# Optimization experiments

Measured on AMD Instinct MI355X. Metric: run time of the kernel, lower is better.

## Reference

```python
import jax, jax.numpy as jnp
import numpy as np

B, N, D = 2, 256, 128
LN_EPS = 1e-5


def _linear_params(key, d, scale):
    kw, kb = jax.random.split(key)
    W = jax.random.normal(kw, (d, d), jnp.float32) * scale
    b = jax.random.normal(kb, (d,), jnp.float32) * 0.02
    return W, b


def setup_inputs() -> dict:
    key = jax.random.key(0)
    ks = jax.random.split(key, 8)
    hidden_states = jax.random.normal(ks[0], (B, N, D), jnp.float32)
    structure_matrix = jax.random.normal(ks[1], (B, N, N, D), jnp.float32)
    scale = 1.0 / np.sqrt(D).astype(np.float32)
    Wq, bq = _linear_params(ks[2], D, scale)
    Wk, bk = _linear_params(ks[3], D, scale)
    Wv, bv = _linear_params(ks[4], D, scale)
    Wo, bo = _linear_params(ks[5], D, scale)
    ln_g = jnp.ones((D,), jnp.float32)
    ln_b = jnp.zeros((D,), jnp.float32)
    return dict(hidden_states=hidden_states, structure_matrix=structure_matrix,
                Wq=Wq, bq=bq, Wk=Wk, bk=bk, Wv=Wv, bv=bv, Wo=Wo, bo=bo,
                ln_g=ln_g, ln_b=ln_b)


def reference(hidden_states, structure_matrix, Wq, bq, Wk, bk, Wv, bv, Wo, bo, ln_g, ln_b):
    # hidden_states is accepted by the original forward but never used.
    d = structure_matrix.shape[-1]
    q = structure_matrix @ Wq + bq  # [B,N,N,D]
    k = structure_matrix @ Wk + bk
    v = structure_matrix @ Wv + bv
    # scores[b,i,j,k] = <Q[b,i,k,:], K[b,i,j,:]> / sqrt(D)
    # (equivalent to the torch broadcast multiply+sum, expressed as batched GEMM)
    scores = jnp.einsum('bikd,bijd->bijk', q, k) / jnp.sqrt(jnp.asarray(d, scores_dtype := q.dtype))
    probs = jax.nn.relu(scores)  # dropout is identity in eval mode
    # context[b,i,j,d] = sum_k probs[b,i,j,k] * V[b,i,k,d]
    ctx = jnp.einsum('bijk,bikd->bijd', probs, v)
    out = ctx @ Wo + bo
    x = out + structure_matrix  # residual
    mu = jnp.mean(x, axis=-1, keepdims=True)
    var = jnp.var(x, axis=-1, keepdims=True)
    return (x - mu) * jax.lax.rsqrt(var + LN_EPS) * ln_g + ln_b
```

## Files before the change

kernel.cpp:

```cpp
#include <hip/hip_runtime.h>

#define DEV static __device__ __forceinline__

typedef __bf16 bf16x8 __attribute__((ext_vector_type(8)));
typedef float  f32x16 __attribute__((ext_vector_type(16)));

DEV int rowmap(int r, int hi) { return (r & 3) + 8 * (r >> 2) + 4 * hi; }

DEV int swzQ(int row, int col) {
  return row * 256 + (((((col >> 3) ^ (row & 15)) << 3) | (col & 7)) << 1);
}
DEV int swzV(int d, int k) {
  return d * 512 + (((((k >> 3) ^ (d & 31)) << 3) | (k & 7)) << 1);
}

DEV unsigned pack2(float lo, float hi) {
  union { __bf16 h[2]; unsigned u; } x;
  x.h[0] = (__bf16)lo; x.h[1] = (__bf16)hi;
  return x.u;
}

DEV bf16x8 mk_frag(float d0, float d1, float d2, float d3,
                   float d4, float d5, float d6, float d7, int lane) {
  unsigned a0 = pack2(d0, d1), a1 = pack2(d2, d3);
  unsigned b0 = pack2(d4, d5), b1 = pack2(d6, d7);
  unsigned a0s = __shfl_xor(a0, 32), a1s = __shfl_xor(a1, 32);
  unsigned b0s = __shfl_xor(b0, 32), b1s = __shfl_xor(b1, 32);
  bool lo = lane < 32;
  union { unsigned u[4]; bf16x8 v; } r;
  r.u[0] = lo ? a0  : b0s;
  r.u[1] = lo ? a1  : b1s;
  r.u[2] = lo ? a0s : b0;
  r.u[3] = lo ? a1s : b1;
  return r.v;
}

DEV f32x16 fzero() {
  f32x16 z;
  #pragma unroll
  for (int i = 0; i < 16; ++i) z[i] = 0.f;
  return z;
}

DEV void gld16(const char* g, char* l) {
  __builtin_amdgcn_global_load_lds(
      (const __attribute__((address_space(1))) void*)g,
      (__attribute__((address_space(3))) void*)l, 16, 0, 0);
}

DEV void stage_w32(const float* __restrict__ W, char* dst, int tid) {
  #pragma unroll
  for (int it = 0; it < 32; ++it) {
    int idx = tid + it * 512;
    int e = idx >> 7, dp = idx & 127;
    *reinterpret_cast<__bf16*>(dst + swzQ(dp, e)) = (__bf16)W[idx];
  }
}

__global__ void prep_wt(const float* __restrict__ Wk, const float* __restrict__ Wq,
                        const float* __restrict__ Wv, const float* __restrict__ Wo,
                        __bf16* __restrict__ wt) {
  int idx = blockIdx.x * 256 + threadIdx.x;
  const float* W[4] = {Wk, Wq, Wv, Wo};
  int m = idx >> 14, rem = idx & 16383;
  int e = rem >> 7, dp = rem & 127;
  wt[m * 16384 + (swzQ(dp, e) >> 1)] = (__bf16)W[m][rem];
}

template<bool WS>
__global__ __launch_bounds__(512, 2)
void sapd_fused(const float* __restrict__ S,
                const float* __restrict__ bq, const float* __restrict__ bk,
                const float* __restrict__ bv, const float* __restrict__ bo,
                const float* __restrict__ Wq, const float* __restrict__ Wk,
                const float* __restrict__ Wv, const float* __restrict__ Wo,
                const float* __restrict__ lg, const float* __restrict__ lb,
                const __bf16* __restrict__ wt,
                float* __restrict__ out)
{
  extern __shared__ char smem[];
  char* RA = smem;
  char* RB = smem + 65536;

  const int tid  = threadIdx.x;
  const int lane = tid & 63;
  const int w    = tid >> 6;
  const int ml   = lane & 31;
  const int hi   = lane >> 5;
  const size_t sbase = (size_t)blockIdx.x * (256 * 128);
  const char* wsc = (const char*)wt;

  if (WS) {
    #pragma unroll
    for (int j = 0; j < 12; ++j) {
      int c = w + 8 * j;
      char* dst = (c < 64) ? (RB + c * 1024) : (RA + (c - 64) * 1024);
      gld16(wsc + c * 1024 + lane * 16, dst);
    }
  } else {
    stage_w32(Wk, RB, tid);
    stage_w32(Wq, RB + 32768, tid);
    stage_w32(Wv, RA, tid);
  }

  bf16x8 sfrag[8];
  {
    const float* srow = S + sbase + (size_t)(32 * w + ml) * 128;
    #pragma unroll
    for (int kk = 0; kk < 8; ++kk) {
      float4 a = *reinterpret_cast<const float4*>(srow + 16 * kk + 8 * hi);
      float4 b = *reinterpret_cast<const float4*>(srow + 16 * kk + 8 * hi + 4);
      bf16x8 f;
      f[0] = (__bf16)a.x; f[1] = (__bf16)a.y; f[2] = (__bf16)a.z; f[3] = (__bf16)a.w;
      f[4] = (__bf16)b.x; f[5] = (__bf16)b.y; f[6] = (__bf16)b.z; f[7] = (__bf16)b.w;
      sfrag[kk] = f;
    }
  }
  __syncthreads();

  bf16x8 kfrag[8];
  {
    f32x16 accK[4];
    #pragma unroll
    for (int t = 0; t < 4; ++t) accK[t] = fzero();
    #pragma unroll
    for (int kk = 0; kk < 8; ++kk) {
      #pragma unroll
      for (int t = 0; t < 4; ++t) {
        bf16x8 wf = *reinterpret_cast<const bf16x8*>(
            RB + swzQ(32 * t + ml, 16 * kk + 8 * hi));
        accK[t] = __builtin_amdgcn_mfma_f32_32x32x16_bf16(wf, sfrag[kk], accK[t], 0, 0, 0);
      }
    }
    #pragma unroll
    for (int t = 0; t < 4; ++t) {
      #pragma unroll
      for (int r = 0; r < 16; ++r) accK[t][r] += bk[32 * t + rowmap(r, hi)];
      kfrag[2 * t]     = mk_frag(accK[t][0], accK[t][1], accK[t][2], accK[t][3],
                                 accK[t][4], accK[t][5], accK[t][6], accK[t][7], lane);
      kfrag[2 * t + 1] = mk_frag(accK[t][8], accK[t][9], accK[t][10], accK[t][11],
                                 accK[t][12], accK[t][13], accK[t][14], accK[t][15], lane);
    }
  }

  {
    f32x16 accV[4];
    #pragma unroll
    for (int t = 0; t < 4; ++t) accV[t] = fzero();
    #pragma unroll
    for (int kk = 0; kk < 8; ++kk) {
      #pragma unroll
      for (int t = 0; t < 4; ++t) {
        bf16x8 wf = *reinterpret_cast<const bf16x8*>(
            RA + swzQ(32 * t + ml, 16 * kk + 8 * hi));
        accV[t] = __builtin_amdgcn_mfma_f32_32x32x16_bf16(sfrag[kk], wf, accV[t], 0, 0, 0);
      }
    }
    __syncthreads();
    #pragma unroll
    for (int t = 0; t < 4; ++t) {
      float bb = bv[32 * t + ml];
      int d = 32 * t + ml;
      #pragma unroll
      for (int p = 0; p < 8; ++p) {
        int k = 32 * w + rowmap(2 * p, hi);
        *reinterpret_cast<unsigned*>(RA + swzV(d, k)) =
            pack2(accV[t][2 * p] + bb, accV[t][2 * p + 1] + bb);
      }
    }
  }

  {
    f32x16 accQ[4];
    #pragma unroll
    for (int t = 0; t < 4; ++t) accQ[t] = fzero();
    #pragma unroll
    for (int kk = 0; kk < 8; ++kk) {
      #pragma unroll
      for (int t = 0; t < 4; ++t) {
        bf16x8 wf = *reinterpret_cast<const bf16x8*>(
            RB + 32768 + swzQ(32 * t + ml, 16 * kk + 8 * hi));
        accQ[t] = __builtin_amdgcn_mfma_f32_32x32x16_bf16(sfrag[kk], wf, accQ[t], 0, 0, 0);
      }
    }
    __syncthreads();
    #pragma unroll
    for (int t = 0; t < 4; ++t) {
      float bb = bq[32 * t + ml];
      #pragma unroll
      for (int r = 0; r < 16; ++r)
        *reinterpret_cast<__bf16*>(
            RB + swzQ(32 * w + rowmap(r, hi), 32 * t + ml)) =
            (__bf16)(accQ[t][r] + bb);
    }
  }
  __syncthreads();

  f32x16 ctx[4];
  #pragma unroll
  for (int m = 0; m < 4; ++m) ctx[m] = fzero();
  const float SC = 0.088388347648318447f;

  #pragma unroll 2
  for (int kt = 0; kt < 8; ++kt) {
    f32x16 sa = fzero();
    __builtin_amdgcn_s_setprio(1);
    #pragma unroll
    for (int kk = 0; kk < 8; ++kk) {
      bf16x8 qf = *reinterpret_cast<const bf16x8*>(
          RB + swzQ(32 * kt + ml, 16 * kk + 8 * hi));
      sa = __builtin_amdgcn_mfma_f32_32x32x16_bf16(qf, kfrag[kk], sa, 0, 0, 0);
    }
    __builtin_amdgcn_s_setprio(0);
    float p[16];
    #pragma unroll
    for (int r = 0; r < 16; ++r) p[r] = fmaxf(sa[r] * SC, 0.f);
    bf16x8 pf0 = mk_frag(p[0], p[1], p[2], p[3], p[4], p[5], p[6], p[7], lane);
    bf16x8 pf1 = mk_frag(p[8], p[9], p[10], p[11], p[12], p[13], p[14], p[15], lane);
    __builtin_amdgcn_s_setprio(1);
    #pragma unroll
    for (int m = 0; m < 4; ++m) {
      bf16x8 vf0 = *reinterpret_cast<const bf16x8*>(
          RA + swzV(32 * m + ml, 32 * kt + 8 * hi));
      ctx[m] = __builtin_amdgcn_mfma_f32_32x32x16_bf16(vf0, pf0, ctx[m], 0, 0, 0);
      bf16x8 vf1 = *reinterpret_cast<const bf16x8*>(
          RA + swzV(32 * m + ml, 32 * kt + 16 + 8 * hi));
      ctx[m] = __builtin_amdgcn_mfma_f32_32x32x16_bf16(vf1, pf1, ctx[m], 0, 0, 0);
    }
    __builtin_amdgcn_s_setprio(0);

    if (kt == 3) {
      __syncthreads();
      if (WS) {
        #pragma unroll
        for (int j = 0; j < 4; ++j) {
          int c = w + 8 * j;
          gld16(wsc + 98304 + c * 1024 + lane * 16, RB + c * 1024);
        }
      } else {
        stage_w32(Wo, RB, tid);
      }
    }
  }

  bf16x8 cf[8];
  #pragma unroll
  for (int m = 0; m < 4; ++m) {
    cf[2 * m]     = mk_frag(ctx[m][0], ctx[m][1], ctx[m][2], ctx[m][3],
                            ctx[m][4], ctx[m][5], ctx[m][6], ctx[m][7], lane);
    cf[2 * m + 1] = mk_frag(ctx[m][8], ctx[m][9], ctx[m][10], ctx[m][11],
                            ctx[m][12], ctx[m][13], ctx[m][14], ctx[m][15], lane);
  }
  float resv[4][16];
  #pragma unroll
  for (int t = 0; t < 4; ++t) {
    #pragma unroll
    for (int r = 0; r < 16; ++r)
      resv[t][r] = S[sbase + (size_t)(32 * w + rowmap(r, hi)) * 128 + 32 * t + ml];
  }
  __syncthreads();

  f32x16 oa[4];
  #pragma unroll
  for (int t = 0; t < 4; ++t) oa[t] = fzero();
  #pragma unroll
  for (int kk = 0; kk < 8; ++kk) {
    #pragma unroll
    for (int t = 0; t < 4; ++t) {
      bf16x8 wf = *reinterpret_cast<const bf16x8*>(
          RB + swzQ(32 * t + ml, 16 * kk + 8 * hi));
      oa[t] = __builtin_amdgcn_mfma_f32_32x32x16_bf16(cf[kk], wf, oa[t], 0, 0, 0);
    }
  }

  float gg[4], lbv[4], bov[4];
  #pragma unroll
  for (int t = 0; t < 4; ++t) {
    gg[t]  = lg[32 * t + ml];
    lbv[t] = lb[32 * t + ml];
    bov[t] = bo[32 * t + ml];
  }
  float sum[16], ssq[16];
  #pragma unroll
  for (int r = 0; r < 16; ++r) { sum[r] = 0.f; ssq[r] = 0.f; }
  #pragma unroll
  for (int t = 0; t < 4; ++t) {
    #pragma unroll
    for (int r = 0; r < 16; ++r) {
      float x = oa[t][r] + bov[t] + resv[t][r];
      oa[t][r] = x;
      sum[r] += x;
      ssq[r] += x * x;
    }
  }
  #pragma unroll
  for (int r = 0; r < 16; ++r) {
    float s_ = sum[r], q_ = ssq[r];
    #pragma unroll
    for (int m = 1; m <= 16; m <<= 1) {
      s_ += __shfl_xor(s_, m);
      q_ += __shfl_xor(q_, m);
    }
    float mu = s_ * (1.f / 128.f);
    float var = q_ * (1.f / 128.f) - mu * mu;
    float rs = rsqrtf(var + 1e-5f);
    float* orow = out + sbase + (size_t)(32 * w + rowmap(r, hi)) * 128;
    #pragma unroll
    for (int t = 0; t < 4; ++t)
      orow[32 * t + ml] = (oa[t][r] - mu) * rs * gg[t] + lbv[t];
  }
}

extern "C" void kernel_launch(void* const* d_in, const int* in_sizes, int n_in,
                              void* d_out, int out_size, void* d_ws, size_t ws_size,
                              hipStream_t stream) {
  (void)in_sizes; (void)n_in; (void)out_size;
  const float* S  = (const float*)d_in[1];
  const float* Wq = (const float*)d_in[2];
  const float* bq = (const float*)d_in[3];
  const float* Wk = (const float*)d_in[4];
  const float* bk = (const float*)d_in[5];
  const float* Wv = (const float*)d_in[6];
  const float* bv = (const float*)d_in[7];
  const float* Wo = (const float*)d_in[8];
  const float* bo = (const float*)d_in[9];
  const float* lg = (const float*)d_in[10];
  const float* lb = (const float*)d_in[11];
  float* out = (float*)d_out;

  constexpr int SMEM = 131072;
  bool use_ws = (d_ws != nullptr) && (ws_size >= 131072);
  if (use_ws) {
    prep_wt<<<dim3(256), dim3(256), 0, stream>>>(Wk, Wq, Wv, Wo, (__bf16*)d_ws);
    (void)hipFuncSetAttribute(reinterpret_cast<const void*>(&sapd_fused<true>),
                              hipFuncAttributeMaxDynamicSharedMemorySize, SMEM);
    sapd_fused<true><<<dim3(512), dim3(512), SMEM, stream>>>(
        S, bq, bk, bv, bo, Wq, Wk, Wv, Wo, lg, lb, (const __bf16*)d_ws, out);
  } else {
    (void)hipFuncSetAttribute(reinterpret_cast<const void*>(&sapd_fused<false>),
                              hipFuncAttributeMaxDynamicSharedMemorySize, SMEM);
    sapd_fused<false><<<dim3(512), dim3(512), SMEM, stream>>>(
        S, bq, bk, bv, bo, Wq, Wk, Wv, Wo, lg, lb, nullptr, out);
  }
}
```

Measured before the change: 72.79 us.

## Split each row tile across two waves with 1024-thread blocks

Result: slower. 144.0 us (+97.8%).

```diff
diff --git a/kernel.cpp b/kernel.cpp
--- a/kernel.cpp
+++ b/kernel.cpp
@@ -19,6 +19,8 @@
   x.h[0] = (__bf16)lo; x.h[1] = (__bf16)hi;
   return x.u;
 }
+DEV float bflo(unsigned u) { union { unsigned u; float f; } x; x.u = u << 16;        return x.f; }
+DEV float bfhi(unsigned u) { union { unsigned u; float f; } x; x.u = u & 0xffff0000u; return x.f; }
 
 DEV bf16x8 mk_frag(float d0, float d1, float d2, float d3,
                    float d4, float d5, float d6, float d7, int lane) {
@@ -50,8 +52,8 @@
 
 DEV void stage_w32(const float* __restrict__ W, char* dst, int tid) {
   #pragma unroll
-  for (int it = 0; it < 32; ++it) {
-    int idx = tid + it * 512;
+  for (int it = 0; it < 16; ++it) {
+    int idx = tid + it * 1024;
     int e = idx >> 7, dp = idx & 127;
     *reinterpret_cast<__bf16*>(dst + swzQ(dp, e)) = (__bf16)W[idx];
   }
@@ -68,7 +70,7 @@
 }
 
 template<bool WS>
-__global__ __launch_bounds__(512, 2)
+__global__ __launch_bounds__(1024, 4)
 void sapd_fused(const float* __restrict__ S,
                 const float* __restrict__ bq, const float* __restrict__ bk,
                 const float* __restrict__ bv, const float* __restrict__ bo,
@@ -85,6 +87,8 @@
   const int tid  = threadIdx.x;
   const int lane = tid & 63;
   const int w    = tid >> 6;
+  const int p    = w >> 1;
+  const int s    = w & 1;
   const int ml   = lane & 31;
   const int hi   = lane >> 5;
   const size_t sbase = (size_t)blockIdx.x * (256 * 128);
@@ -92,20 +96,22 @@
 
   if (WS) {
     #pragma unroll
-    for (int j = 0; j < 12; ++j) {
-      int c = w + 8 * j;
-      char* dst = (c < 64) ? (RB + c * 1024) : (RA + (c - 64) * 1024);
+    for (int jj = 0; jj < 6; ++jj) {
+      int c = w + 16 * jj;
+      char* dst = (c < 32) ? (RA + c * 1024)
+                : (c < 64) ? (RB + (c - 32) * 1024)
+                           : (RA + 32768 + (c - 64) * 1024);
       gld16(wsc + c * 1024 + lane * 16, dst);
     }
   } else {
-    stage_w32(Wk, RB, tid);
-    stage_w32(Wq, RB + 32768, tid);
-    stage_w32(Wv, RA, tid);
+    stage_w32(Wk, RA, tid);
+    stage_w32(Wq, RB, tid);
+    stage_w32(Wv, RA + 32768, tid);
   }
 
   bf16x8 sfrag[8];
   {
-    const float* srow = S + sbase + (size_t)(32 * w + ml) * 128;
+    const float* srow = S + sbase + (size_t)(32 * p + ml) * 128;
     #pragma unroll
     for (int kk = 0; kk < 8; ++kk) {
       float4 a = *reinterpret_cast<const float4*>(srow + 16 * kk + 8 * hi);
@@ -128,7 +134,7 @@
       #pragma unroll
       for (int t = 0; t < 4; ++t) {
         bf16x8 wf = *reinterpret_cast<const bf16x8*>(
-            RB + swzQ(32 * t + ml, 16 * kk + 8 * hi));
+            RA + swzQ(32 * t + ml, 16 * kk + 8 * hi));
         accK[t] = __builtin_amdgcn_mfma_f32_32x32x16_bf16(wf, sfrag[kk], accK[t], 0, 0, 0);
       }
     }
@@ -143,56 +149,54 @@
     }
   }
 
-  {
-    f32x16 accV[4];
-    #pragma unroll
-    for (int t = 0; t < 4; ++t) accV[t] = fzero();
-    #pragma unroll
-    for (int kk = 0; kk < 8; ++kk) {
-      #pragma unroll
-      for (int t = 0; t < 4; ++t) {
-        bf16x8 wf = *reinterpret_cast<const bf16x8*>(
-            RA + swzQ(32 * t + ml, 16 * kk + 8 * hi));
-        accV[t] = __builtin_amdgcn_mfma_f32_32x32x16_bf16(sfrag[kk], wf, accV[t], 0, 0, 0);
-      }
-    }
-    __syncthreads();
-    #pragma unroll
-    for (int t = 0; t < 4; ++t) {
-      float bb = bv[32 * t + ml];
-      int d = 32 * t + ml;
-      #pragma unroll
-      for (int p = 0; p < 8; ++p) {
-        int k = 32 * w + rowmap(2 * p, hi);
-        *reinterpret_cast<unsigned*>(RA + swzV(d, k)) =
-            pack2(accV[t][2 * p] + bb, accV[t][2 * p + 1] + bb);
-      }
-    }
-  }
-
-  {
-    f32x16 accQ[4];
-    #pragma unroll
-    for (int t = 0; t < 4; ++t) accQ[t] = fzero();
-    #pragma unroll
-    for (int kk = 0; kk < 8; ++kk) {
-      #pragma unroll
-      for (int t = 0; t < 4; ++t) {
-        bf16x8 wf = *reinterpret_cast<const bf16x8*>(
-            RB + 32768 + swzQ(32 * t + ml, 16 * kk + 8 * hi));
-        accQ[t] = __builtin_amdgcn_mfma_f32_32x32x16_bf16(sfrag[kk], wf, accQ[t], 0, 0, 0);
-      }
-    }
-    __syncthreads();
-    #pragma unroll
-    for (int t = 0; t < 4; ++t) {
-      float bb = bq[32 * t + ml];
-      #pragma unroll
-      for (int r = 0; r < 16; ++r)
-        *reinterpret_cast<__bf16*>(
-            RB + swzQ(32 * w + rowmap(r, hi), 32 * t + ml)) =
-            (__bf16)(accQ[t][r] + bb);
-    }
+  f32x16 accV[2];
+  accV[0] = fzero(); accV[1] = fzero();
+  #pragma unroll
+  for (int kk = 0; kk < 8; ++kk) {
+    #pragma unroll
+    for (int tt = 0; tt < 2; ++tt) {
+      int t = 2 * s + tt;
+      bf16x8 wf = *reinterpret_cast<const bf16x8*>(
+          RA + 32768 + swzQ(32 * t + ml, 16 * kk + 8 * hi));
+      accV[tt] = __builtin_amdgcn_mfma_f32_32x32x16_bf16(sfrag[kk], wf, accV[tt], 0, 0, 0);
+    }
+  }
+
+  f32x16 accQ[2];
+  accQ[0] = fzero(); accQ[1] = fzero();
+  #pragma unroll
+  for (int kk = 0; kk < 8; ++kk) {
+    #pragma unroll
+    for (int tt = 0; tt < 2; ++tt) {
+      int t = 2 * s + tt;
+      bf16x8 wf = *reinterpret_cast<const bf16x8*>(
+          RB + swzQ(32 * t + ml, 16 * kk + 8 * hi));
+      accQ[tt] = __builtin_amdgcn_mfma_f32_32x32x16_bf16(sfrag[kk], wf, accQ[tt], 0, 0, 0);
+    }
+  }
+  __syncthreads();
+
+  #pragma unroll
+  for (int tt = 0; tt < 2; ++tt) {
+    int t = 2 * s + tt;
+    float bb = bv[32 * t + ml];
+    int d = 32 * t + ml;
+    #pragma unroll
+    for (int q = 0; q < 8; ++q) {
+      int k = 32 * p + rowmap(2 * q, hi);
+      *reinterpret_cast<unsigned*>(RA + swzV(d, k)) =
+          pack2(accV[tt][2 * q] + bb, accV[tt][2 * q + 1] + bb);
+    }
+  }
+  #pragma unroll
+  for (int tt = 0; tt < 2; ++tt) {
+    int t = 2 * s + tt;
+    float bb = bq[32 * t + ml];
+    #pragma unroll
+    for (int r = 0; r < 16; ++r)
+      *reinterpret_cast<__bf16*>(
+          RB + swzQ(32 * p + rowmap(r, hi), 32 * t + ml)) =
+          (__bf16)(accQ[tt][r] + bb);
   }
   __syncthreads();
 
@@ -201,8 +205,9 @@
   for (int m = 0; m < 4; ++m) ctx[m] = fzero();
   const float SC = 0.088388347648318447f;
 
-  #pragma unroll 2
-  for (int kt = 0; kt < 8; ++kt) {
+  #pragma unroll
+  for (int c = 0; c < 4; ++c) {
+    int kt = 4 * s + c;
     f32x16 sa = fzero();
     __builtin_amdgcn_s_setprio(1);
     #pragma unroll
@@ -212,11 +217,11 @@
       sa = __builtin_amdgcn_mfma_f32_32x32x16_bf16(qf, kfrag[kk], sa, 0, 0, 0);
     }
     __builtin_amdgcn_s_setprio(0);
-    float p[16];
-    #pragma unroll
-    for (int r = 0; r < 16; ++r) p[r] = fmaxf(sa[r] * SC, 0.f);
-    bf16x8 pf0 = mk_frag(p[0], p[1], p[2], p[3], p[4], p[5], p[6], p[7], lane);
-    bf16x8 pf1 = mk_frag(p[8], p[9], p[10], p[11], p[12], p[13], p[14], p[15], lane);
+    float pv[16];
+    #pragma unroll
+    for (int r = 0; r < 16; ++r) pv[r] = fmaxf(sa[r] * SC, 0.f);
+    bf16x8 pf0 = mk_frag(pv[0], pv[1], pv[2], pv[3], pv[4], pv[5], pv[6], pv[7], lane);
+    bf16x8 pf1 = mk_frag(pv[8], pv[9], pv[10], pv[11], pv[12], pv[13], pv[14], pv[15], lane);
     __builtin_amdgcn_s_setprio(1);
     #pragma unroll
     for (int m = 0; m < 4; ++m) {
@@ -228,17 +233,62 @@
       ctx[m] = __builtin_amdgcn_mfma_f32_32x32x16_bf16(vf1, pf1, ctx[m], 0, 0, 0);
     }
     __builtin_amdgcn_s_setprio(0);
-
-    if (kt == 3) {
-      __syncthreads();
-      if (WS) {
-        #pragma unroll
-        for (int j = 0; j < 4; ++j) {
-          int c = w + 8 * j;
-          gld16(wsc + 98304 + c * 1024 + lane * 16, RB + c * 1024);
-        }
-      } else {
-        stage_w32(Wo, RB, tid);
+  }
+  __syncthreads();
+
+  if (WS) {
+    #pragma unroll
+    for (int jj = 0; jj < 2; ++jj) {
+      int c = w + 16 * jj;
+      gld16(wsc + 98304 + c * 1024 + lane * 16, RB + c * 1024);
+    }
+  } else {
+    stage_w32(Wo, RB, tid);
+  }
+  char* XC = RA + p * 8192;
+  if (s == 1) {
+    #pragma unroll
+    for (int m = 0; m < 4; ++m) {
+      #pragma unroll
+      for (int q = 0; q < 8; ++q) {
+        int d2 = (32 * m + rowmap(2 * q, hi)) >> 1;
+        *reinterpret_cast<unsigned*>(XC + d2 * 128 + ml * 4) =
+            pack2(ctx[m][2 * q], ctx[m][2 * q + 1]);
+      }
+    }
+  }
+  __syncthreads();
+  if (s == 0) {
+    #pragma unroll
+    for (int m = 0; m < 4; ++m) {
+      #pragma unroll
+      for (int q = 0; q < 8; ++q) {
+        int d2 = (32 * m + rowmap(2 * q, hi)) >> 1;
+        unsigned u = *reinterpret_cast<unsigned*>(XC + d2 * 128 + ml * 4);
+        ctx[m][2 * q]     += bflo(u);
+        ctx[m][2 * q + 1] += bfhi(u);
+      }
+    }
+    #pragma unroll
+    for (int m = 0; m < 4; ++m) {
+      #pragma unroll
+      for (int q = 0; q < 8; ++q) {
+        int d2 = (32 * m + rowmap(2 * q, hi)) >> 1;
+        *reinterpret_cast<unsigned*>(XC + d2 * 128 + ml * 4) =
+            pack2(ctx[m][2 * q], ctx[m][2 * q + 1]);
+      }
+    }
+  }
+  __syncthreads();
+  if (s == 1) {
+    #pragma unroll
+    for (int m = 0; m < 4; ++m) {
+      #pragma unroll
+      for (int q = 0; q < 8; ++q) {
+        int d2 = (32 * m + rowmap(2 * q, hi)) >> 1;
+        unsigned u = *reinterpret_cast<unsigned*>(XC + d2 * 128 + ml * 4);
+        ctx[m][2 * q]     = bflo(u);
+        ctx[m][2 * q + 1] = bfhi(u);
       }
     }
   }
@@ -251,48 +301,50 @@
     cf[2 * m + 1] = mk_frag(ctx[m][8], ctx[m][9], ctx[m][10], ctx[m][11],
                             ctx[m][12], ctx[m][13], ctx[m][14], ctx[m][15], lane);
   }
-  float resv[4][16];
-  #pragma unroll
-  for (int t = 0; t < 4; ++t) {
+  float resv[2][16];
+  #pragma unroll
+  for (int tt = 0; tt < 2; ++tt) {
     #pragma unroll
     for (int r = 0; r < 16; ++r)
-      resv[t][r] = S[sbase + (size_t)(32 * w + rowmap(r, hi)) * 128 + 32 * t + ml];
-  }
-  __syncthreads();
-
-  f32x16 oa[4];
-  #pragma unroll
-  for (int t = 0; t < 4; ++t) oa[t] = fzero();
+      resv[tt][r] = S[sbase + (size_t)(32 * p + rowmap(r, hi)) * 128 +
+                      32 * (2 * s + tt) + ml];
+  }
+
+  f32x16 oa[2];
+  oa[0] = fzero(); oa[1] = fzero();
   #pragma unroll
   for (int kk = 0; kk < 8; ++kk) {
     #pragma unroll
-    for (int t = 0; t < 4; ++t) {
+    for (int tt = 0; tt < 2; ++tt) {
+      int t = 2 * s + tt;
       bf16x8 wf = *reinterpret_cast<const bf16x8*>(
           RB + swzQ(32 * t + ml, 16 * kk + 8 * hi));
-      oa[t] = __builtin_amdgcn_mfma_f32_32x32x16_bf16(cf[kk], wf, oa[t], 0, 0, 0);
-    }
-  }
-
-  float gg[4], lbv[4], bov[4];
-  #pragma unroll
-  for (int t = 0; t < 4; ++t) {
-    gg[t]  = lg[32 * t + ml];
-    lbv[t] = lb[32 * t + ml];
-    bov[t] = bo[32 * t + ml];
+      oa[tt] = __builtin_amdgcn_mfma_f32_32x32x16_bf16(cf[kk], wf, oa[tt], 0, 0, 0);
+    }
+  }
+
+  float gg[2], lbv[2], bov[2];
+  #pragma unroll
+  for (int tt = 0; tt < 2; ++tt) {
+    int t = 2 * s + tt;
+    gg[tt]  = lg[32 * t + ml];
+    lbv[tt] = lb[32 * t + ml];
+    bov[tt] = bo[32 * t + ml];
   }
   float sum[16], ssq[16];
   #pragma unroll
   for (int r = 0; r < 16; ++r) { sum[r] = 0.f; ssq[r] = 0.f; }
   #pragma unroll
-  for (int t = 0; t < 4; ++t) {
+  for (int tt = 0; tt < 2; ++tt) {
     #pragma unroll
     for (int r = 0; r < 16; ++r) {
-      float x = oa[t][r] + bov[t] + resv[t][r];
-      oa[t][r] = x;
+      float x = oa[tt][r] + bov[tt] + resv[tt][r];
+      oa[tt][r] = x;
       sum[r] += x;
       ssq[r] += x * x;
     }
   }
+  char* SX = RB + 32768;
   #pragma unroll
   for (int r = 0; r < 16; ++r) {
     float s_ = sum[r], q_ = ssq[r];
@@ -301,13 +353,24 @@
       s_ += __shfl_xor(s_, m);
       q_ += __shfl_xor(q_, m);
     }
-    float mu = s_ * (1.f / 128.f);
-    float var = q_ * (1.f / 128.f) - mu * mu;
+    if (ml == 0) {
+      float2 v; v.x = s_; v.y = q_;
+      *reinterpret_cast<float2*>(SX + p * 512 + rowmap(r, hi) * 16 + s * 8) = v;
+    }
+  }
+  __syncthreads();
+  #pragma unroll
+  for (int r = 0; r < 16; ++r) {
+    int row = rowmap(r, hi);
+    float2 a = *reinterpret_cast<float2*>(SX + p * 512 + row * 16);
+    float2 b = *reinterpret_cast<float2*>(SX + p * 512 + row * 16 + 8);
+    float mu = (a.x + b.x) * (1.f / 128.f);
+    float var = (a.y + b.y) * (1.f / 128.f) - mu * mu;
     float rs = rsqrtf(var + 1e-5f);
-    float* orow = out + sbase + (size_t)(32 * w + rowmap(r, hi)) * 128;
-    #pragma unroll
-    for (int t = 0; t < 4; ++t)
-      orow[32 * t + ml] = (oa[t][r] - mu) * rs * gg[t] + lbv[t];
+    float* orow = out + sbase + (size_t)(32 * p + row) * 128;
+    #pragma unroll
+    for (int tt = 0; tt < 2; ++tt)
+      orow[32 * (2 * s + tt) + ml] = (oa[tt][r] - mu) * rs * gg[tt] + lbv[tt];
   }
 }
 
@@ -334,12 +397,12 @@
     prep_wt<<<dim3(256), dim3(256), 0, stream>>>(Wk, Wq, Wv, Wo, (__bf16*)d_ws);
     (void)hipFuncSetAttribute(reinterpret_cast<const void*>(&sapd_fused<true>),
                               hipFuncAttributeMaxDynamicSharedMemorySize, SMEM);
-    sapd_fused<true><<<dim3(512), dim3(512), SMEM, stream>>>(
+    sapd_fused<true><<<dim3(512), dim3(1024), SMEM, stream>>>(
         S, bq, bk, bv, bo, Wq, Wk, Wv, Wo, lg, lb, (const __bf16*)d_ws, out);
   } else {
     (void)hipFuncSetAttribute(reinterpret_cast<const void*>(&sapd_fused<false>),
                               hipFuncAttributeMaxDynamicSharedMemorySize, SMEM);
-    sapd_fused<false><<<dim3(512), dim3(512), SMEM, stream>>>(
+    sapd_fused<false><<<dim3(512), dim3(1024), SMEM, stream>>>(
         S, bq, bk, bv, bo, Wq, Wk, Wv, Wo, lg, lb, nullptr, out);
   }
 }
```

## Fold Q/K and V/O weight products algebraically to skip per-tile projections

Applied to the files above, without the earlier changes.

New measurement: 233.7 us. 221% more time.

```diff
diff --git a/kernel.cpp b/kernel.cpp
--- a/kernel.cpp
+++ b/kernel.cpp
@@ -9,9 +9,6 @@
 
 DEV int swzQ(int row, int col) {
   return row * 256 + (((((col >> 3) ^ (row & 15)) << 3) | (col & 7)) << 1);
-}
-DEV int swzV(int d, int k) {
-  return d * 512 + (((((k >> 3) ^ (d & 31)) << 3) | (k & 7)) << 1);
 }
 
 DEV unsigned pack2(float lo, float hi) {
@@ -48,39 +45,82 @@
       (__attribute__((address_space(3))) void*)l, 16, 0, 0);
 }
 
-DEV void stage_w32(const float* __restrict__ W, char* dst, int tid) {
-  #pragma unroll
-  for (int it = 0; it < 32; ++it) {
-    int idx = tid + it * 512;
-    int e = idx >> 7, dp = idx & 127;
-    *reinterpret_cast<__bf16*>(dst + swzQ(dp, e)) = (__bf16)W[idx];
-  }
-}
-
-__global__ void prep_wt(const float* __restrict__ Wk, const float* __restrict__ Wq,
-                        const float* __restrict__ Wv, const float* __restrict__ Wo,
-                        __bf16* __restrict__ wt) {
-  int idx = blockIdx.x * 256 + threadIdx.x;
-  const float* W[4] = {Wk, Wq, Wv, Wo};
-  int m = idx >> 14, rem = idx & 16383;
-  int e = rem >> 7, dp = rem & 127;
-  wt[m * 16384 + (swzQ(dp, e) >> 1)] = (__bf16)W[m][rem];
-}
-
-template<bool WS>
+DEV void st_write(char* SB, int colbase, const bf16x8 sf[8], int ml, int hi) {
+  #pragma unroll
+  for (int kk = 0; kk < 8; ++kk) {
+    union { bf16x8 v; unsigned u[4]; } o, q;
+    o.v = sf[kk];
+    #pragma unroll
+    for (int x = 0; x < 4; ++x) q.u[x] = __shfl_xor(o.u[x], 1);
+    bool even = ((ml & 1) == 0);
+    if (even ? (kk < 4) : (kk >= 4)) {
+      int col = colbase + (ml & ~1);
+      #pragma unroll
+      for (int i = 0; i < 8; ++i) {
+        int e = 16 * kk + 8 * hi + i;
+        union { __bf16 h[2]; unsigned u; } pk;
+        pk.h[0] = even ? o.v[i] : q.v[i];
+        pk.h[1] = even ? q.v[i] : o.v[i];
+        *reinterpret_cast<unsigned*>(SB + swzQ(e, col)) = pk.u;
+      }
+    }
+  }
+}
+
+__global__ void prep_mat(const float* __restrict__ X, const float* __restrict__ Y,
+                         char* __restrict__ dst, int transx) {
+  extern __shared__ char pm[];
+  float* yl = reinterpret_cast<float*>(pm);
+  float* xl = yl + 128 * 129;
+  int t = threadIdx.x;
+  int a0 = blockIdx.x * 16;
+  for (int i = t; i < 16384; i += 256) yl[(i >> 7) * 129 + (i & 127)] = Y[i];
+  for (int i = t; i < 2048; i += 256) {
+    int aa = i >> 7, d = i & 127;
+    xl[aa * 129 + d] = transx ? X[d * 128 + a0 + aa] : X[(a0 + aa) * 128 + d];
+  }
+  __syncthreads();
+  int b = t & 127, ah = t >> 7;
+  #pragma unroll
+  for (int aa = 0; aa < 8; ++aa) {
+    int a = ah * 8 + aa;
+    float acc = 0.f;
+    for (int d = 0; d < 128; ++d) acc += xl[a * 129 + d] * yl[b * 129 + d];
+    *reinterpret_cast<__bf16*>(dst + swzQ(a0 + a, b)) = (__bf16)acc;
+  }
+}
+
+__global__ void prep_v(const float* __restrict__ Wq, const float* __restrict__ Wk,
+                       const float* __restrict__ Wo,
+                       const float* __restrict__ bq, const float* __restrict__ bk,
+                       const float* __restrict__ bv, float* __restrict__ dstf) {
+  int e = threadIdx.x;
+  float a1 = 0.f, a2 = 0.f, a3 = 0.f;
+  for (int d = 0; d < 128; ++d) {
+    a1 += Wq[e * 128 + d] * bk[d];
+    a2 += Wk[e * 128 + d] * bq[d];
+    a3 += bv[d] * Wo[d * 128 + e];
+  }
+  dstf[e] = a1; dstf[128 + e] = a2; dstf[256 + e] = a3;
+  if (e == 0) {
+    float c = 0.f;
+    for (int d = 0; d < 128; ++d) c += bq[d] * bk[d];
+    dstf[384] = c;
+  }
+}
+
 __global__ __launch_bounds__(512, 2)
 void sapd_fused(const float* __restrict__ S,
-                const float* __restrict__ bq, const float* __restrict__ bk,
-                const float* __restrict__ bv, const float* __restrict__ bo,
-                const float* __restrict__ Wq, const float* __restrict__ Wk,
-                const float* __restrict__ Wv, const float* __restrict__ Wo,
+                const float* __restrict__ bo,
                 const float* __restrict__ lg, const float* __restrict__ lb,
-                const __bf16* __restrict__ wt,
+                const char* __restrict__ ws,
                 float* __restrict__ out)
 {
   extern __shared__ char smem[];
-  char* RA = smem;
-  char* RB = smem + 65536;
+  char* SA = smem;
+  char* SB = smem + 32768;
+  float* a_lds  = reinterpret_cast<float*>(smem + 65536);
+  float* rs_lds = a_lds + 256;
 
   const int tid  = threadIdx.x;
   const int lane = tid & 63;
@@ -88,19 +128,12 @@
   const int ml   = lane & 31;
   const int hi   = lane >> 5;
   const size_t sbase = (size_t)blockIdx.x * (256 * 128);
-  const char* wsc = (const char*)wt;
-
-  if (WS) {
-    #pragma unroll
-    for (int j = 0; j < 12; ++j) {
-      int c = w + 8 * j;
-      char* dst = (c < 64) ? (RB + c * 1024) : (RA + (c - 64) * 1024);
-      gld16(wsc + c * 1024 + lane * 16, dst);
-    }
-  } else {
-    stage_w32(Wk, RB, tid);
-    stage_w32(Wq, RB + 32768, tid);
-    stage_w32(Wv, RA, tid);
+  const float* wsf = reinterpret_cast<const float*>(ws + 65536);
+
+  #pragma unroll
+  for (int j = 0; j < 4; ++j) {
+    int c = w + 8 * j;
+    gld16(ws + c * 1024 + lane * 16, SA + c * 1024);
   }
 
   bf16x8 sfrag[8];
@@ -116,140 +149,144 @@
       sfrag[kk] = f;
     }
   }
-  __syncthreads();
-
-  bf16x8 kfrag[8];
+
+  if (w < 4) st_write(SB, 32 * w, sfrag, ml, hi);
+  __syncthreads();
+
+  bf16x8 rfrag[8];
   {
-    f32x16 accK[4];
-    #pragma unroll
-    for (int t = 0; t < 4; ++t) accK[t] = fzero();
+    f32x16 racc[4];
+    #pragma unroll
+    for (int t = 0; t < 4; ++t) racc[t] = fzero();
     #pragma unroll
     for (int kk = 0; kk < 8; ++kk) {
       #pragma unroll
       for (int t = 0; t < 4; ++t) {
-        bf16x8 wf = *reinterpret_cast<const bf16x8*>(
-            RB + swzQ(32 * t + ml, 16 * kk + 8 * hi));
-        accK[t] = __builtin_amdgcn_mfma_f32_32x32x16_bf16(wf, sfrag[kk], accK[t], 0, 0, 0);
+        bf16x8 gf = *reinterpret_cast<const bf16x8*>(
+            SA + swzQ(32 * t + ml, 16 * kk + 8 * hi));
+        racc[t] = __builtin_amdgcn_mfma_f32_32x32x16_bf16(gf, sfrag[kk], racc[t], 0, 0, 0);
       }
     }
     #pragma unroll
     for (int t = 0; t < 4; ++t) {
-      #pragma unroll
-      for (int r = 0; r < 16; ++r) accK[t][r] += bk[32 * t + rowmap(r, hi)];
-      kfrag[2 * t]     = mk_frag(accK[t][0], accK[t][1], accK[t][2], accK[t][3],
-                                 accK[t][4], accK[t][5], accK[t][6], accK[t][7], lane);
-      kfrag[2 * t + 1] = mk_frag(accK[t][8], accK[t][9], accK[t][10], accK[t][11],
-                                 accK[t][12], accK[t][13], accK[t][14], accK[t][15], lane);
-    }
-  }
-
+      rfrag[2 * t]     = mk_frag(racc[t][0], racc[t][1], racc[t][2], racc[t][3],
+                                 racc[t][4], racc[t][5], racc[t][6], racc[t][7], lane);
+      rfrag[2 * t + 1] = mk_frag(racc[t][8], racc[t][9], racc[t][10], racc[t][11],
+                                 racc[t][12], racc[t][13], racc[t][14], racc[t][15], lane);
+    }
+  }
+
+  float c_own;
   {
-    f32x16 accV[4];
-    #pragma unroll
-    for (int t = 0; t < 4; ++t) accV[t] = fzero();
+    f32x16 sa2 = fzero();
     #pragma unroll
     for (int kk = 0; kk < 8; ++kk) {
-      #pragma unroll
-      for (int t = 0; t < 4; ++t) {
-        bf16x8 wf = *reinterpret_cast<const bf16x8*>(
-            RA + swzQ(32 * t + ml, 16 * kk + 8 * hi));
-        accV[t] = __builtin_amdgcn_mfma_f32_32x32x16_bf16(sfrag[kk], wf, accV[t], 0, 0, 0);
-      }
-    }
-    __syncthreads();
-    #pragma unroll
-    for (int t = 0; t < 4; ++t) {
-      float bb = bv[32 * t + ml];
-      int d = 32 * t + ml;
-      #pragma unroll
-      for (int p = 0; p < 8; ++p) {
-        int k = 32 * w + rowmap(2 * p, hi);
-        *reinterpret_cast<unsigned*>(RA + swzV(d, k)) =
-            pack2(accV[t][2 * p] + bb, accV[t][2 * p + 1] + bb);
-      }
+      bf16x8 vmf;
+      if (ml < 2) {
+        const float* vp = wsf + (ml == 0 ? 128 : 0);
+        #pragma unroll
+        for (int i = 0; i < 8; ++i) vmf[i] = (__bf16)vp[16 * kk + 8 * hi + i];
+      } else {
+        #pragma unroll
+        for (int i = 0; i < 8; ++i) vmf[i] = (__bf16)0.f;
+      }
+      sa2 = __builtin_amdgcn_mfma_f32_32x32x16_bf16(vmf, sfrag[kk], sa2, 0, 0, 0);
+    }
+    float cst = wsf[384];
+    if (hi == 0) a_lds[32 * w + ml] = sa2[1] + cst;
+    c_own = __shfl(sa2[0], ml);
+  }
+  __syncthreads();
+
+  if (w < 4) {
+    #pragma unroll
+    for (int kk = 0; kk < 8; ++kk)
+      *reinterpret_cast<bf16x8*>(SA + swzQ(32 * w + ml, 16 * kk + 8 * hi)) = sfrag[kk];
+  }
+  __syncthreads();
+
+  const float SC = 0.088388347648318447f;
+  f32x16 uacc[4];
+  #pragma unroll
+  for (int m = 0; m < 4; ++m) uacc[m] = fzero();
+  float rs = 0.f;
+
+  #pragma unroll
+  for (int half = 0; half < 2; ++half) {
+    #pragma unroll
+    for (int c4 = 0; c4 < 4; ++c4) {
+      int kt = 4 * half + c4;
+      f32x16 sa = fzero();
+      __builtin_amdgcn_s_setprio(1);
+      #pragma unroll
+      for (int kk = 0; kk < 8; ++kk) {
+        bf16x8 sr = *reinterpret_cast<const bf16x8*>(
+            SA + swzQ(32 * c4 + ml, 16 * kk + 8 * hi));
+        sa = __builtin_amdgcn_mfma_f32_32x32x16_bf16(sr, rfrag[kk], sa, 0, 0, 0);
+      }
+      __builtin_amdgcn_s_setprio(0);
+      float p[16];
+      #pragma unroll
+      for (int r = 0; r < 16; ++r) {
+        float av = a_lds[32 * kt + rowmap(r, hi)];
+        p[r] = fmaxf((sa[r] + av + c_own) * SC, 0.f);
+        rs += p[r];
+      }
+      bf16x8 pf0 = mk_frag(p[0], p[1], p[2], p[3], p[4], p[5], p[6], p[7], lane);
+      bf16x8 pf1 = mk_frag(p[8], p[9], p[10], p[11], p[12], p[13], p[14], p[15], lane);
+      __builtin_amdgcn_s_setprio(1);
+      #pragma unroll
+      for (int m = 0; m < 4; ++m) {
+        bf16x8 st0 = *reinterpret_cast<const bf16x8*>(
+            SB + swzQ(32 * m + ml, 32 * c4 + 8 * hi));
+        uacc[m] = __builtin_amdgcn_mfma_f32_32x32x16_bf16(st0, pf0, uacc[m], 0, 0, 0);
+        bf16x8 st1 = *reinterpret_cast<const bf16x8*>(
+            SB + swzQ(32 * m + ml, 32 * c4 + 16 + 8 * hi));
+        uacc[m] = __builtin_amdgcn_mfma_f32_32x32x16_bf16(st1, pf1, uacc[m], 0, 0, 0);
+      }
+      __builtin_amdgcn_s_setprio(0);
+    }
+    if (half == 0) {
+      __syncthreads();
+      if (w >= 4) {
+        bf16x8 tf[8];
+        const float* srow = S + sbase + (size_t)(32 * w + ml) * 128;
+        #pragma unroll
+        for (int kk = 0; kk < 8; ++kk) {
+          float4 a = *reinterpret_cast<const float4*>(srow + 16 * kk + 8 * hi);
+          float4 b = *reinterpret_cast<const float4*>(srow + 16 * kk + 8 * hi + 4);
+          bf16x8 f;
+          f[0] = (__bf16)a.x; f[1] = (__bf16)a.y; f[2] = (__bf16)a.z; f[3] = (__bf16)a.w;
+          f[4] = (__bf16)b.x; f[5] = (__bf16)b.y; f[6] = (__bf16)b.z; f[7] = (__bf16)b.w;
+          tf[kk] = f;
+        }
+        st_write(SB, 32 * (w - 4), tf, ml, hi);
+        #pragma unroll
+        for (int kk = 0; kk < 8; ++kk)
+          *reinterpret_cast<bf16x8*>(
+              SA + swzQ(32 * (w - 4) + ml, 16 * kk + 8 * hi)) = tf[kk];
+      }
+      __syncthreads();
     }
   }
 
   {
-    f32x16 accQ[4];
-    #pragma unroll
-    for (int t = 0; t < 4; ++t) accQ[t] = fzero();
-    #pragma unroll
-    for (int kk = 0; kk < 8; ++kk) {
-      #pragma unroll
-      for (int t = 0; t < 4; ++t) {
-        bf16x8 wf = *reinterpret_cast<const bf16x8*>(
-            RB + 32768 + swzQ(32 * t + ml, 16 * kk + 8 * hi));
-        accQ[t] = __builtin_amdgcn_mfma_f32_32x32x16_bf16(sfrag[kk], wf, accQ[t], 0, 0, 0);
-      }
-    }
-    __syncthreads();
-    #pragma unroll
-    for (int t = 0; t < 4; ++t) {
-      float bb = bq[32 * t + ml];
-      #pragma unroll
-      for (int r = 0; r < 16; ++r)
-        *reinterpret_cast<__bf16*>(
-            RB + swzQ(32 * w + rowmap(r, hi), 32 * t + ml)) =
-            (__bf16)(accQ[t][r] + bb);
-    }
-  }
-  __syncthreads();
-
-  f32x16 ctx[4];
-  #pragma unroll
-  for (int m = 0; m < 4; ++m) ctx[m] = fzero();
-  const float SC = 0.088388347648318447f;
-
-  #pragma unroll 2
-  for (int kt = 0; kt < 8; ++kt) {
-    f32x16 sa = fzero();
-    __builtin_amdgcn_s_setprio(1);
-    #pragma unroll
-    for (int kk = 0; kk < 8; ++kk) {
-      bf16x8 qf = *reinterpret_cast<const bf16x8*>(
-          RB + swzQ(32 * kt + ml, 16 * kk + 8 * hi));
-      sa = __builtin_amdgcn_mfma_f32_32x32x16_bf16(qf, kfrag[kk], sa, 0, 0, 0);
-    }
-    __builtin_amdgcn_s_setprio(0);
-    float p[16];
-    #pragma unroll
-    for (int r = 0; r < 16; ++r) p[r] = fmaxf(sa[r] * SC, 0.f);
-    bf16x8 pf0 = mk_frag(p[0], p[1], p[2], p[3], p[4], p[5], p[6], p[7], lane);
-    bf16x8 pf1 = mk_frag(p[8], p[9], p[10], p[11], p[12], p[13], p[14], p[15], lane);
-    __builtin_amdgcn_s_setprio(1);
-    #pragma unroll
-    for (int m = 0; m < 4; ++m) {
-      bf16x8 vf0 = *reinterpret_cast<const bf16x8*>(
-          RA + swzV(32 * m + ml, 32 * kt + 8 * hi));
-      ctx[m] = __builtin_amdgcn_mfma_f32_32x32x16_bf16(vf0, pf0, ctx[m], 0, 0, 0);
-      bf16x8 vf1 = *reinterpret_cast<const bf16x8*>(
-          RA + swzV(32 * m + ml, 32 * kt + 16 + 8 * hi));
-      ctx[m] = __builtin_amdgcn_mfma_f32_32x32x16_bf16(vf1, pf1, ctx[m], 0, 0, 0);
-    }
-    __builtin_amdgcn_s_setprio(0);
-
-    if (kt == 3) {
-      __syncthreads();
-      if (WS) {
-        #pragma unroll
-        for (int j = 0; j < 4; ++j) {
-          int c = w + 8 * j;
-          gld16(wsc + 98304 + c * 1024 + lane * 16, RB + c * 1024);
-        }
-      } else {
-        stage_w32(Wo, RB, tid);
-      }
-    }
-  }
-
+    float rs2 = rs + __shfl_xor(rs, 32);
+    if (hi == 0) rs_lds[32 * w + ml] = rs2;
+  }
+  __syncthreads();
+  #pragma unroll
+  for (int j = 0; j < 4; ++j) {
+    int c = w + 8 * j;
+    gld16(ws + 32768 + c * 1024 + lane * 16, SA + c * 1024);
+  }
   bf16x8 cf[8];
   #pragma unroll
   for (int m = 0; m < 4; ++m) {
-    cf[2 * m]     = mk_frag(ctx[m][0], ctx[m][1], ctx[m][2], ctx[m][3],
-                            ctx[m][4], ctx[m][5], ctx[m][6], ctx[m][7], lane);
-    cf[2 * m + 1] = mk_frag(ctx[m][8], ctx[m][9], ctx[m][10], ctx[m][11],
-                            ctx[m][12], ctx[m][13], ctx[m][14], ctx[m][15], lane);
+    cf[2 * m]     = mk_frag(uacc[m][0], uacc[m][1], uacc[m][2], uacc[m][3],
+                            uacc[m][4], uacc[m][5], uacc[m][6], uacc[m][7], lane);
+    cf[2 * m + 1] = mk_frag(uacc[m][8], uacc[m][9], uacc[m][10], uacc[m][11],
+                            uacc[m][12], uacc[m][13], uacc[m][14], uacc[m][15], lane);
   }
   float resv[4][16];
   #pragma unroll
@@ -267,19 +304,24 @@
   for (int kk = 0; kk < 8; ++kk) {
     #pragma unroll
     for (int t = 0; t < 4; ++t) {
-      bf16x8 wf = *reinterpret_cast<const bf16x8*>(
-          RB + swzQ(32 * t + ml, 16 * kk + 8 * hi));
-      oa[t] = __builtin_amdgcn_mfma_f32_32x32x16_bf16(cf[kk], wf, oa[t], 0, 0, 0);
-    }
-  }
-
-  float gg[4], lbv[4], bov[4];
+      bf16x8 hf = *reinterpret_cast<const bf16x8*>(
+          SA + swzQ(32 * t + ml, 16 * kk + 8 * hi));
+      oa[t] = __builtin_amdgcn_mfma_f32_32x32x16_bf16(cf[kk], hf, oa[t], 0, 0, 0);
+    }
+  }
+
+  float gg[4], lbv[4], bov[4], w2v[4];
   #pragma unroll
   for (int t = 0; t < 4; ++t) {
     gg[t]  = lg[32 * t + ml];
     lbv[t] = lb[32 * t + ml];
     bov[t] = bo[32 * t + ml];
-  }
+    w2v[t] = wsf[256 + 32 * t + ml];
+  }
+  float rsr[16];
+  #pragma unroll
+  for (int r = 0; r < 16; ++r) rsr[r] = rs_lds[32 * w + rowmap(r, hi)];
+
   float sum[16], ssq[16];
   #pragma unroll
   for (int r = 0; r < 16; ++r) { sum[r] = 0.f; ssq[r] = 0.f; }
@@ -287,7 +329,7 @@
   for (int t = 0; t < 4; ++t) {
     #pragma unroll
     for (int r = 0; r < 16; ++r) {
-      float x = oa[t][r] + bov[t] + resv[t][r];
+      float x = oa[t][r] + rsr[r] * w2v[t] + bov[t] + resv[t][r];
       oa[t][r] = x;
       sum[r] += x;
       ssq[r] += x * x;
@@ -303,18 +345,18 @@
     }
     float mu = s_ * (1.f / 128.f);
     float var = q_ * (1.f / 128.f) - mu * mu;
-    float rs = rsqrtf(var + 1e-5f);
+    float rq = rsqrtf(var + 1e-5f);
     float* orow = out + sbase + (size_t)(32 * w + rowmap(r, hi)) * 128;
     #pragma unroll
     for (int t = 0; t < 4; ++t)
-      orow[32 * t + ml] = (oa[t][r] - mu) * rs * gg[t] + lbv[t];
+      orow[32 * t + ml] = (oa[t][r] - mu) * rq * gg[t] + lbv[t];
   }
 }
 
 extern "C" void kernel_launch(void* const* d_in, const int* in_sizes, int n_in,
                               void* d_out, int out_size, void* d_ws, size_t ws_size,
                               hipStream_t stream) {
-  (void)in_sizes; (void)n_in; (void)out_size;
+  (void)in_sizes; (void)n_in; (void)out_size; (void)ws_size;
   const float* S  = (const float*)d_in[1];
   const float* Wq = (const float*)d_in[2];
   const float* bq = (const float*)d_in[3];
@@ -327,19 +369,18 @@
   const float* lg = (const float*)d_in[10];
   const float* lb = (const float*)d_in[11];
   float* out = (float*)d_out;
-
-  constexpr int SMEM = 131072;
-  bool use_ws = (d_ws != nullptr) && (ws_size >= 131072);
-  if (use_ws) {
-    prep_wt<<<dim3(256), dim3(256), 0, stream>>>(Wk, Wq, Wv, Wo, (__bf16*)d_ws);
-    (void)hipFuncSetAttribute(reinterpret_cast<const void*>(&sapd_fused<true>),
-                              hipFuncAttributeMaxDynamicSharedMemorySize, SMEM);
-    sapd_fused<true><<<dim3(512), dim3(512), SMEM, stream>>>(
-        S, bq, bk, bv, bo, Wq, Wk, Wv, Wo, lg, lb, (const __bf16*)d_ws, out);
-  } else {
-    (void)hipFuncSetAttribute(reinterpret_cast<const void*>(&sapd_fused<false>),
-                              hipFuncAttributeMaxDynamicSharedMemorySize, SMEM);
-    sapd_fused<false><<<dim3(512), dim3(512), SMEM, stream>>>(
-        S, bq, bk, bv, bo, Wq, Wk, Wv, Wo, lg, lb, nullptr, out);
-  }
-}
+  char* ws = (char*)d_ws;
+
+  constexpr int PSM = (128 * 129 + 16 * 129) * 4;
+  (void)hipFuncSetAttribute(reinterpret_cast<const void*>(&prep_mat),
+                            hipFuncAttributeMaxDynamicSharedMemorySize, PSM);
+  prep_mat<<<dim3(8), dim3(256), PSM, stream>>>(Wq, Wk, ws, 0);
+  prep_mat<<<dim3(8), dim3(256), PSM, stream>>>(Wo, Wv, ws + 32768, 1);
+  prep_v<<<dim3(1), dim3(128), 0, stream>>>(Wq, Wk, Wo, bq, bk, bv,
+                                            (float*)(ws + 65536));
+
+  constexpr int SMEM = 67584;
+  (void)hipFuncSetAttribute(reinterpret_cast<const void*>(&sapd_fused),
+                            hipFuncAttributeMaxDynamicSharedMemorySize, SMEM);
+  sapd_fused<<<dim3(512), dim3(512), SMEM, stream>>>(S, bo, lg, lb, ws, out);
+}
```
